# Kernel tuning notes

Measured on AMD Instinct MI355X. Metric: run time of the kernel, lower is better.

The kernel has to match this reference:

```python
import jax, jax.numpy as jnp
import numpy as np

EMB, HID, SEQ, BATCH, VOCAB, LAYERS = 1024, 1024, 128, 64, 10000, 2


def setup_inputs() -> dict:
    key = jax.random.key(0)
    ks = jax.random.split(key, 10)
    k = 1.0 / np.sqrt(HID)
    u = lambda kk, shape, lo, hi: jax.random.uniform(kk, shape, jnp.float32, lo, hi)
    return {
        "inputs": jax.random.randint(ks[0], (SEQ, BATCH), 0, VOCAB, jnp.int32),
        "hidden": jnp.zeros((LAYERS, BATCH, HID), jnp.float32),
        "embedding": u(ks[1], (VOCAB, EMB), -0.1, 0.1),
        "wx0": u(ks[2], (HID, EMB), -k, k),
        "wh0": u(ks[3], (HID, HID), -k, k),
        "bh0": u(ks[4], (HID,), -k, k),
        "wx1": u(ks[5], (HID, HID), -k, k),
        "wh1": u(ks[6], (HID, HID), -k, k),
        "bh1": u(ks[7], (HID,), -k, k),
        "v_w": u(ks[8], (VOCAB, HID), -0.1, 0.1),
        "v_b": jnp.zeros((VOCAB,), jnp.float32),
    }


def reference(inputs, hidden, embedding, wx0, wh0, bh0, wx1, wh1, bh1, v_w, v_b):
    # dropout is identity (dp_keep_prob = 1.0)
    emb = embedding[inputs]  # (S, B, E)

    def step(h, x_t):
        # h: (L, B, H); x_t: (B, E)
        h0 = jnp.tanh(x_t @ wx0.T + h[0] @ wh0.T + bh0)
        h1 = jnp.tanh(h0 @ wx1.T + h[1] @ wh1.T + bh1)
        return jnp.stack([h0, h1]), h1

    hidden_final, top = jax.lax.scan(step, hidden, emb)  # top: (S, B, H)
    logits = jnp.einsum("sbh,vh->sbv", top, v_w) + v_b  # (S, B, V)
    return logits, hidden_final
```

## Files before the change

kernel.cpp:

```cpp
#include <hip/hip_runtime.h>
#include <stdint.h>

typedef __attribute__((ext_vector_type(8))) short short8;
typedef __attribute__((ext_vector_type(4))) float f32x4;
typedef __attribute__((ext_vector_type(4))) unsigned short ushort4v;
typedef __attribute__((ext_vector_type(4))) float float4v;

#define DEVFN static __device__ __forceinline__
#define SPIN_CAP (1u << 20)

DEVFN unsigned short f32_to_bf16_rn(float x) {
  unsigned u = __builtin_bit_cast(unsigned, x);
  unsigned r = u + 0x7FFFu + ((u >> 16) & 1u);
  return (unsigned short)(r >> 16);
}
DEVFN float bf16_to_f32(unsigned short h) {
  unsigned u = ((unsigned)h) << 16;
  return __builtin_bit_cast(float, u);
}

__global__ void k_split(const float* __restrict__ src, unsigned short* __restrict__ hi,
                        unsigned short* __restrict__ lo, int n) {
  int i = (blockIdx.x * 256 + threadIdx.x) * 4;
  if (i >= n) return;
  float4v v = *reinterpret_cast<const float4v*>(src + i);
  ushort4v h, l;
#pragma unroll
  for (int j = 0; j < 4; ++j) {
    unsigned short hb = f32_to_bf16_rn(v[j]);
    float rem = v[j] - bf16_to_f32(hb);
    h[j] = hb;
    l[j] = f32_to_bf16_rn(rem);
  }
  *reinterpret_cast<ushort4v*>(hi + i) = h;
  *reinterpret_cast<ushort4v*>(lo + i) = l;
}

__global__ void k_embed(const int* __restrict__ tok, const float* __restrict__ emb,
                        unsigned short* __restrict__ hi, unsigned short* __restrict__ lo) {
  int m = blockIdx.x;
  int t = tok[m];
  const float* row = emb + (size_t)t * 1024;
  int e = threadIdx.x * 4;
  float4v v = *reinterpret_cast<const float4v*>(row + e);
  ushort4v h, l;
#pragma unroll
  for (int j = 0; j < 4; ++j) {
    unsigned short hb = f32_to_bf16_rn(v[j]);
    float rem = v[j] - bf16_to_f32(hb);
    h[j] = hb;
    l[j] = f32_to_bf16_rn(rem);
  }
  *reinterpret_cast<ushort4v*>(hi + (size_t)m * 1024 + e) = h;
  *reinterpret_cast<ushort4v*>(lo + (size_t)m * 1024 + e) = l;
}

template <bool NGUARD>
__global__ __launch_bounds__(256) void k_gemm_nt(
    const unsigned short* __restrict__ Ahi, const unsigned short* __restrict__ Alo,
    const unsigned short* __restrict__ Bhi, const unsigned short* __restrict__ Blo,
    float* __restrict__ C, const float* __restrict__ bias, int N) {
  const int K = 1024;
  __shared__ unsigned short sA[2][128][40];
  __shared__ unsigned short sB[2][128][40];
  const int m0 = blockIdx.y * 128;
  const int n0 = blockIdx.x * 128;
  const int tid = threadIdx.x;
  const int lane = tid & 63, wave = tid >> 6;
  const int wm = (wave >> 1) * 64, wn = (wave & 1) * 64;
  const int fr = lane & 15, fk = (lane >> 4) * 8, fm = (lane >> 4) * 4;

  f32x4 acc[4][4] = {};

  for (int k0 = 0; k0 < K; k0 += 32) {
    __syncthreads();
#pragma unroll
    for (int a = 0; a < 2; ++a) {
      const unsigned short* As = a ? Alo : Ahi;
      const unsigned short* Bs = a ? Blo : Bhi;
#pragma unroll
      for (int p = 0; p < 2; ++p) {
        int seg = p * 256 + tid;
        int row = seg >> 2, sk = (seg & 3) * 8;
        short8 va = *reinterpret_cast<const short8*>(As + (size_t)(m0 + row) * K + k0 + sk);
        *reinterpret_cast<short8*>(&sA[a][row][sk]) = va;
        short8 vb;
        if (!NGUARD || (n0 + row) < N)
          vb = *reinterpret_cast<const short8*>(Bs + (size_t)(n0 + row) * K + k0 + sk);
        else
          vb = short8{0, 0, 0, 0, 0, 0, 0, 0};
        *reinterpret_cast<short8*>(&sB[a][row][sk]) = vb;
      }
    }
    __syncthreads();

    short8 afh[4], afl[4], bfh[4], bfl[4];
#pragma unroll
    for (int i = 0; i < 4; ++i) {
      afh[i] = *reinterpret_cast<const short8*>(&sA[0][wm + i * 16 + fr][fk]);
      afl[i] = *reinterpret_cast<const short8*>(&sA[1][wm + i * 16 + fr][fk]);
      bfh[i] = *reinterpret_cast<const short8*>(&sB[0][wn + i * 16 + fr][fk]);
      bfl[i] = *reinterpret_cast<const short8*>(&sB[1][wn + i * 16 + fr][fk]);
    }
#pragma unroll
    for (int i = 0; i < 4; ++i)
#pragma unroll
      for (int j = 0; j < 4; ++j) {
        acc[i][j] = __builtin_amdgcn_mfma_f32_16x16x32_bf16(afh[i], bfh[j], acc[i][j], 0, 0, 0);
        acc[i][j] = __builtin_amdgcn_mfma_f32_16x16x32_bf16(afl[i], bfh[j], acc[i][j], 0, 0, 0);
        acc[i][j] = __builtin_amdgcn_mfma_f32_16x16x32_bf16(afh[i], bfl[j], acc[i][j], 0, 0, 0);
      }
  }

#pragma unroll
  for (int i = 0; i < 4; ++i)
#pragma unroll
    for (int j = 0; j < 4; ++j) {
      int n = n0 + wn + j * 16 + fr;
      if (NGUARD && n >= N) continue;
      float bv = bias[n];
#pragma unroll
      for (int r = 0; r < 4; ++r) {
        int m = m0 + wm + i * 16 + fm + r;
        C[(size_t)m * N + n] = acc[i][j][r] + bv;
      }
    }
}

#define NWG_L0 32
#define NWG_CMP 96

DEVFN f32x4 MFMA(short8 a, short8 b, f32x4 c) {
  return __builtin_amdgcn_mfma_f32_16x16x32_bf16(a, b, c, 0, 0, 0);
}

__global__ __launch_bounds__(256, 1) void k_rnn_fused(
    const float* __restrict__ X0,
    unsigned short* __restrict__ H0hi, unsigned short* __restrict__ H0lo,
    unsigned short* __restrict__ H1hi, unsigned short* __restrict__ H1lo,
    const unsigned short* __restrict__ Wh0hi, const unsigned short* __restrict__ Wh0lo,
    const unsigned short* __restrict__ Wx1hi, const unsigned short* __restrict__ Wx1lo,
    const unsigned short* __restrict__ Wh1hi, const unsigned short* __restrict__ Wh1lo,
    const float* __restrict__ bh1,
    unsigned* __restrict__ slots, unsigned* __restrict__ release) {
  const int wg = blockIdx.x;
  const int tid = threadIdx.x;

  if (wg == NWG_CMP) {
    if (tid >= 64) return;
    const int lane = tid;
    for (int i = 0; i < 129; ++i) {
      unsigned want = (unsigned)(i + 1);
      for (unsigned sp = 0; sp < SPIN_CAP; ++sp) {
        unsigned a = __hip_atomic_load(&slots[lane * 32], __ATOMIC_RELAXED,
                                       __HIP_MEMORY_SCOPE_AGENT);
        unsigned b = (lane < 32) ? __hip_atomic_load(&slots[(64 + lane) * 32], __ATOMIC_RELAXED,
                                                     __HIP_MEMORY_SCOPE_AGENT)
                                 : 0xFFFFFFFFu;
        if (__all(a >= want && b >= want)) break;
        __builtin_amdgcn_s_sleep(1);
      }
      if (lane == 0)
        __hip_atomic_store(release, want, __ATOMIC_RELAXED, __HIP_MEMORY_SCOPE_AGENT);
    }
    return;
  }

  const int lane = tid & 63, kw = tid >> 6;
  const int fr = lane & 15, fk = (lane >> 4) * 8;
  const int pr = (lane >> 4) * 4;
  const bool isL0 = wg < NWG_L0;
  __shared__ float red[4][64][36];

  short8 bh_[2][8], bl_[2][8];
  int n0;
  if (isL0) {
    n0 = wg * 32;
#pragma unroll
    for (int cf = 0; cf < 2; ++cf)
#pragma unroll
      for (int ch = 0; ch < 8; ++ch) {
        size_t off = (size_t)(n0 + cf * 16 + fr) * 1024 + kw * 256 + ch * 32 + fk;
        bh_[cf][ch] = *reinterpret_cast<const short8*>(Wh0hi + off);
        bl_[cf][ch] = *reinterpret_cast<const short8*>(Wh0lo + off);
      }
  } else {
    n0 = (wg - NWG_L0) * 16;
#pragma unroll
    for (int ch = 0; ch < 8; ++ch) {
      size_t off = (size_t)(n0 + fr) * 1024 + kw * 256 + ch * 32 + fk;
      bh_[0][ch] = *reinterpret_cast<const short8*>(Wx1hi + off);
      bl_[0][ch] = *reinterpret_cast<const short8*>(Wx1lo + off);
      bh_[1][ch] = *reinterpret_cast<const short8*>(Wh1hi + off);
      bl_[1][ch] = *reinterpret_cast<const short8*>(Wh1lo + off);
    }
  }
  float bias1[4];
  if (!isL0) {
    int cb = (tid & 3) * 4;
#pragma unroll
    for (int c = 0; c < 4; ++c) bias1[c] = bh1[n0 + cb + c];
  }

  for (int i = 0; i <= 128; ++i) {
    const bool active = isL0 ? (i < 128) : (i >= 1);
    if (active) {
      if (isL0) {
        const unsigned short* ah = H0hi + (size_t)i * 65536;
        const unsigned short* al = H0lo + (size_t)i * 65536;
        f32x4 acc[4][2] = {};
#pragma unroll
        for (int ch = 0; ch < 8; ++ch) {
          short8 Ah[4], Al[4];
#pragma unroll
          for (int rf = 0; rf < 4; ++rf) {
            size_t off = (size_t)(rf * 16 + fr) * 1024 + kw * 256 + ch * 32 + fk;
            Ah[rf] = *reinterpret_cast<const short8*>(ah + off);
            Al[rf] = *reinterpret_cast<const short8*>(al + off);
          }
#pragma unroll
          for (int rf = 0; rf < 4; ++rf)
#pragma unroll
            for (int cf = 0; cf < 2; ++cf) {
              acc[rf][cf] = MFMA(Ah[rf], bh_[cf][ch], acc[rf][cf]);
              acc[rf][cf] = MFMA(Al[rf], bh_[cf][ch], acc[rf][cf]);
              acc[rf][cf] = MFMA(Ah[rf], bl_[cf][ch], acc[rf][cf]);
            }
        }
#pragma unroll
        for (int rf = 0; rf < 4; ++rf)
#pragma unroll
          for (int cf = 0; cf < 2; ++cf)
#pragma unroll
            for (int r = 0; r < 4; ++r)
              red[kw][rf * 16 + pr + r][cf * 16 + fr] = acc[rf][cf][r];
      } else {
        const unsigned short* a0h = H0hi + (size_t)i * 65536;
        const unsigned short* a0l = H0lo + (size_t)i * 65536;
        const unsigned short* a1h = H1hi + (size_t)(i - 1) * 65536;
        const unsigned short* a1l = H1lo + (size_t)(i - 1) * 65536;
        f32x4 acc0[4] = {}, acc1[4] = {};
#pragma unroll
        for (int ch = 0; ch < 8; ++ch) {
          short8 A0h[4], A0l[4], A1h[4], A1l[4];
#pragma unroll
          for (int rf = 0; rf < 4; ++rf) {
            size_t off = (size_t)(rf * 16 + fr) * 1024 + kw * 256 + ch * 32 + fk;
            A0h[rf] = *reinterpret_cast<const short8*>(a0h + off);
            A0l[rf] = *reinterpret_cast<const short8*>(a0l + off);
            A1h[rf] = *reinterpret_cast<const short8*>(a1h + off);
            A1l[rf] = *reinterpret_cast<const short8*>(a1l + off);
          }
#pragma unroll
          for (int rf = 0; rf < 4; ++rf) {
            acc0[rf] = MFMA(A0h[rf], bh_[0][ch], acc0[rf]);
            acc0[rf] = MFMA(A0l[rf], bh_[0][ch], acc0[rf]);
            acc0[rf] = MFMA(A0h[rf], bl_[0][ch], acc0[rf]);
            acc1[rf] = MFMA(A1h[rf], bh_[1][ch], acc1[rf]);
            acc1[rf] = MFMA(A1l[rf], bh_[1][ch], acc1[rf]);
            acc1[rf] = MFMA(A1h[rf], bl_[1][ch], acc1[rf]);
          }
        }
#pragma unroll
        for (int rf = 0; rf < 4; ++rf)
#pragma unroll
          for (int r = 0; r < 4; ++r)
            red[kw][rf * 16 + pr + r][fr] = acc0[rf][r] + acc1[rf][r];
      }
      __syncthreads();
      if (isL0) {
        int row = tid >> 2, cb = (tid & 3) * 8;
        const float* Xt = X0 + (size_t)i * 65536 + (size_t)row * 1024 + n0;
        size_t ob = (size_t)(i + 1) * 65536 + (size_t)row * 1024 + n0;
#pragma unroll
        for (int c = 0; c < 8; ++c) {
          int col = cb + c;
          float s = red[0][row][col] + red[1][row][col] + red[2][row][col] + red[3][row][col];
          float val = tanhf(Xt[col] + s);
          unsigned short hb = f32_to_bf16_rn(val);
          float rem = val - bf16_to_f32(hb);
          __hip_atomic_store(H0hi + ob + col, hb, __ATOMIC_RELAXED, __HIP_MEMORY_SCOPE_AGENT);
          __hip_atomic_store(H0lo + ob + col, f32_to_bf16_rn(rem), __ATOMIC_RELAXED,
                             __HIP_MEMORY_SCOPE_AGENT);
        }
      } else {
        int row = tid >> 2, cb = (tid & 3) * 4;
        size_t ob = (size_t)i * 65536 + (size_t)row * 1024 + n0;
#pragma unroll
        for (int c = 0; c < 4; ++c) {
          int col = cb + c;
          float s = red[0][row][col] + red[1][row][col] + red[2][row][col] + red[3][row][col];
          float val = tanhf(bias1[c] + s);
          unsigned short hb = f32_to_bf16_rn(val);
          float rem = val - bf16_to_f32(hb);
          __hip_atomic_store(H1hi + ob + col, hb, __ATOMIC_RELAXED, __HIP_MEMORY_SCOPE_AGENT);
          __hip_atomic_store(H1lo + ob + col, f32_to_bf16_rn(rem), __ATOMIC_RELAXED,
                             __HIP_MEMORY_SCOPE_AGENT);
        }
      }
    }
    __syncthreads();
    if (tid == 0) {
      __hip_atomic_store(&slots[wg * 32], (unsigned)(i + 1), __ATOMIC_RELAXED,
                         __HIP_MEMORY_SCOPE_AGENT);
      for (unsigned sp = 0; sp < SPIN_CAP; ++sp) {
        if (__hip_atomic_load(release, __ATOMIC_RELAXED, __HIP_MEMORY_SCOPE_AGENT) >=
            (unsigned)(i + 1))
          break;
        __builtin_amdgcn_s_sleep(1);
      }
    }
    __syncthreads();
  }
}

__global__ void k_hidfinal(const unsigned short* __restrict__ H0hi,
                           const unsigned short* __restrict__ H0lo,
                           const unsigned short* __restrict__ H1hi,
                           const unsigned short* __restrict__ H1lo,
                           float* __restrict__ out) {
  size_t i = (size_t)blockIdx.x * 256 + threadIdx.x;
  const size_t off = (size_t)128 * 65536;
  out[i] = bf16_to_f32(H0hi[off + i]) + bf16_to_f32(H0lo[off + i]);
  out[65536 + i] = bf16_to_f32(H1hi[off + i]) + bf16_to_f32(H1lo[off + i]);
}

extern "C" void kernel_launch(void* const* d_in, const int* in_sizes, int n_in,
                              void* d_out, int out_size, void* d_ws, size_t ws_size,
                              hipStream_t stream) {
  const int* inputs = (const int*)d_in[0];
  const float* hidden = (const float*)d_in[1];
  const float* emb = (const float*)d_in[2];
  const float* wx0 = (const float*)d_in[3];
  const float* wh0 = (const float*)d_in[4];
  const float* bh0 = (const float*)d_in[5];
  const float* wx1 = (const float*)d_in[6];
  const float* wh1 = (const float*)d_in[7];
  const float* bh1 = (const float*)d_in[8];
  const float* v_w = (const float*)d_in[9];
  const float* v_b = (const float*)d_in[10];
  float* out = (float*)d_out;

  char* ws = (char*)d_ws;
  size_t off = 0;
  auto alloc = [&](size_t bytes) -> char* {
    char* p = ws + off;
    off += (bytes + 255) & ~(size_t)255;
    return p;
  };
  const size_t WB = (size_t)1024 * 1024 * 2;
  unsigned short* wx0hi = (unsigned short*)alloc(WB);
  unsigned short* wx0lo = (unsigned short*)alloc(WB);
  unsigned short* wh0hi = (unsigned short*)alloc(WB);
  unsigned short* wh0lo = (unsigned short*)alloc(WB);
  unsigned short* wx1hi = (unsigned short*)alloc(WB);
  unsigned short* wx1lo = (unsigned short*)alloc(WB);
  unsigned short* wh1hi = (unsigned short*)alloc(WB);
  unsigned short* wh1lo = (unsigned short*)alloc(WB);
  unsigned short* vwhi = (unsigned short*)alloc((size_t)10000 * 1024 * 2);
  unsigned short* vwlo = (unsigned short*)alloc((size_t)10000 * 1024 * 2);
  unsigned short* aehi = (unsigned short*)alloc((size_t)8192 * 1024 * 2);
  unsigned short* aelo = (unsigned short*)alloc((size_t)8192 * 1024 * 2);
  float* X0 = (float*)alloc((size_t)8192 * 1024 * 4);
  const size_t HS = (size_t)129 * 65536 * 2;
  unsigned short* H0hi = (unsigned short*)alloc(HS);
  unsigned short* H0lo = (unsigned short*)alloc(HS);
  unsigned short* H1hi = (unsigned short*)alloc(HS);
  unsigned short* H1lo = (unsigned short*)alloc(HS);
  unsigned* barbuf = (unsigned*)alloc(16384);
  unsigned* slots = barbuf;
  unsigned* release = barbuf + 100 * 32;

  k_split<<<1024, 256, 0, stream>>>(wx0, wx0hi, wx0lo, 1024 * 1024);
  k_split<<<1024, 256, 0, stream>>>(wh0, wh0hi, wh0lo, 1024 * 1024);
  k_split<<<1024, 256, 0, stream>>>(wx1, wx1hi, wx1lo, 1024 * 1024);
  k_split<<<1024, 256, 0, stream>>>(wh1, wh1hi, wh1lo, 1024 * 1024);
  k_split<<<10000, 256, 0, stream>>>(v_w, vwhi, vwlo, 10000 * 1024);
  k_split<<<64, 256, 0, stream>>>(hidden, H0hi, H0lo, 65536);
  k_split<<<64, 256, 0, stream>>>(hidden + 65536, H1hi, H1lo, 65536);
  k_embed<<<8192, 256, 0, stream>>>(inputs, emb, aehi, aelo);
  hipMemsetAsync(barbuf, 0, 16384, stream);

  dim3 g1(8, 64);
  k_gemm_nt<false><<<g1, 256, 0, stream>>>(aehi, aelo, wx0hi, wx0lo, X0, bh0, 1024);

  k_rnn_fused<<<97, 256, 0, stream>>>(X0, H0hi, H0lo, H1hi, H1lo, wh0hi, wh0lo, wx1hi, wx1lo,
                                      wh1hi, wh1lo, bh1, slots, release);

  dim3 g3(79, 64);
  k_gemm_nt<true><<<g3, 256, 0, stream>>>(H1hi + 65536, H1lo + 65536, vwhi, vwlo, out, v_b, 10000);
  k_hidfinal<<<256, 256, 0, stream>>>(H0hi, H0lo, H1hi, H1lo, out + (size_t)81920000);
}
```

Before: 3.704 ms.

## Spread persistent RNN across more workgroups with 8-way K split and sharded release flags

The persistent recurrent kernel grows from 97 to 129 workgroups of 512 threads. Each layer-0 workgroup now owns 16 output columns instead of 32, and K is split across 8 waves instead of 4, so each wave keeps less weight data in registers and does less serial work per step. The single release flag becomes 8 padded copies so pollers are spread across cache lines, and sleep intervals change. The epilogue now packs two bf16 values per 32-bit atomic store. The cost is a larger 8-way LDS reduction and a barrier that has to collect more workgroups each step.

```diff
diff --git a/kernel.cpp b/kernel.cpp
--- a/kernel.cpp
+++ b/kernel.cpp
@@ -5,6 +5,7 @@
 typedef __attribute__((ext_vector_type(4))) float f32x4;
 typedef __attribute__((ext_vector_type(4))) unsigned short ushort4v;
 typedef __attribute__((ext_vector_type(4))) float float4v;
+typedef __attribute__((ext_vector_type(2))) float float2v;
 
 #define DEVFN static __device__ __forceinline__
 #define SPIN_CAP (1u << 20)
@@ -18,6 +19,7 @@
   unsigned u = ((unsigned)h) << 16;
   return __builtin_bit_cast(float, u);
 }
+DEVFN void pin(short8& x) { asm volatile("" : "+v"(*reinterpret_cast<f32x4*>(&x))); }
 
 __global__ void k_split(const float* __restrict__ src, unsigned short* __restrict__ hi,
                         unsigned short* __restrict__ lo, int n) {
@@ -127,14 +129,14 @@
     }
 }
 
-#define NWG_L0 32
-#define NWG_CMP 96
+#define NWG_L0 64
+#define WG_CHK 128
 
 DEVFN f32x4 MFMA(short8 a, short8 b, f32x4 c) {
   return __builtin_amdgcn_mfma_f32_16x16x32_bf16(a, b, c, 0, 0, 0);
 }
 
-__global__ __launch_bounds__(256, 1) void k_rnn_fused(
+__global__ __launch_bounds__(512, 2) void k_rnn_fused(
     const float* __restrict__ X0,
     unsigned short* __restrict__ H0hi, unsigned short* __restrict__ H0lo,
     unsigned short* __restrict__ H1hi, unsigned short* __restrict__ H1lo,
@@ -142,11 +144,11 @@
     const unsigned short* __restrict__ Wx1hi, const unsigned short* __restrict__ Wx1lo,
     const unsigned short* __restrict__ Wh1hi, const unsigned short* __restrict__ Wh1lo,
     const float* __restrict__ bh1,
-    unsigned* __restrict__ slots, unsigned* __restrict__ release) {
+    unsigned* __restrict__ slots, unsigned* __restrict__ releases) {
   const int wg = blockIdx.x;
   const int tid = threadIdx.x;
 
-  if (wg == NWG_CMP) {
+  if (wg == WG_CHK) {
     if (tid >= 64) return;
     const int lane = tid;
     for (int i = 0; i < 129; ++i) {
@@ -154,14 +156,14 @@
       for (unsigned sp = 0; sp < SPIN_CAP; ++sp) {
         unsigned a = __hip_atomic_load(&slots[lane * 32], __ATOMIC_RELAXED,
                                        __HIP_MEMORY_SCOPE_AGENT);
-        unsigned b = (lane < 32) ? __hip_atomic_load(&slots[(64 + lane) * 32], __ATOMIC_RELAXED,
-                                                     __HIP_MEMORY_SCOPE_AGENT)
-                                 : 0xFFFFFFFFu;
+        unsigned b = __hip_atomic_load(&slots[(64 + lane) * 32], __ATOMIC_RELAXED,
+                                       __HIP_MEMORY_SCOPE_AGENT);
         if (__all(a >= want && b >= want)) break;
-        __builtin_amdgcn_s_sleep(1);
-      }
-      if (lane == 0)
-        __hip_atomic_store(release, want, __ATOMIC_RELAXED, __HIP_MEMORY_SCOPE_AGENT);
+        __builtin_amdgcn_s_sleep(2);
+      }
+      if (lane < 8)
+        __hip_atomic_store(&releases[lane * 32], want, __ATOMIC_RELAXED,
+                           __HIP_MEMORY_SCOPE_AGENT);
     }
     return;
   }
@@ -170,82 +172,76 @@
   const int fr = lane & 15, fk = (lane >> 4) * 8;
   const int pr = (lane >> 4) * 4;
   const bool isL0 = wg < NWG_L0;
-  __shared__ float red[4][64][36];
-
-  short8 bh_[2][8], bl_[2][8];
-  int n0;
+  const int n0 = (isL0 ? wg : (wg - NWG_L0)) * 16;
+  __shared__ float red[8][64][20];
+
+  short8 w0h[4], w0l[4], w1h[4], w1l[4];
   if (isL0) {
-    n0 = wg * 32;
-#pragma unroll
-    for (int cf = 0; cf < 2; ++cf)
-#pragma unroll
-      for (int ch = 0; ch < 8; ++ch) {
-        size_t off = (size_t)(n0 + cf * 16 + fr) * 1024 + kw * 256 + ch * 32 + fk;
-        bh_[cf][ch] = *reinterpret_cast<const short8*>(Wh0hi + off);
-        bl_[cf][ch] = *reinterpret_cast<const short8*>(Wh0lo + off);
-      }
+#pragma unroll
+    for (int ch = 0; ch < 4; ++ch) {
+      size_t off = (size_t)(n0 + fr) * 1024 + kw * 128 + ch * 32 + fk;
+      w0h[ch] = *reinterpret_cast<const short8*>(Wh0hi + off);
+      w0l[ch] = *reinterpret_cast<const short8*>(Wh0lo + off);
+      pin(w0h[ch]); pin(w0l[ch]);
+    }
   } else {
-    n0 = (wg - NWG_L0) * 16;
-#pragma unroll
-    for (int ch = 0; ch < 8; ++ch) {
-      size_t off = (size_t)(n0 + fr) * 1024 + kw * 256 + ch * 32 + fk;
-      bh_[0][ch] = *reinterpret_cast<const short8*>(Wx1hi + off);
-      bl_[0][ch] = *reinterpret_cast<const short8*>(Wx1lo + off);
-      bh_[1][ch] = *reinterpret_cast<const short8*>(Wh1hi + off);
-      bl_[1][ch] = *reinterpret_cast<const short8*>(Wh1lo + off);
-    }
-  }
-  float bias1[4];
+#pragma unroll
+    for (int ch = 0; ch < 4; ++ch) {
+      size_t off = (size_t)(n0 + fr) * 1024 + kw * 128 + ch * 32 + fk;
+      w0h[ch] = *reinterpret_cast<const short8*>(Wx1hi + off);
+      w0l[ch] = *reinterpret_cast<const short8*>(Wx1lo + off);
+      w1h[ch] = *reinterpret_cast<const short8*>(Wh1hi + off);
+      w1l[ch] = *reinterpret_cast<const short8*>(Wh1lo + off);
+      pin(w0h[ch]); pin(w0l[ch]); pin(w1h[ch]); pin(w1l[ch]);
+    }
+  }
+  const int row = tid >> 3;
+  const int c0 = (tid & 7) * 2;
+  float bias0 = 0.f, bias1v = 0.f;
   if (!isL0) {
-    int cb = (tid & 3) * 4;
-#pragma unroll
-    for (int c = 0; c < 4; ++c) bias1[c] = bh1[n0 + cb + c];
+    bias0 = bh1[n0 + c0];
+    bias1v = bh1[n0 + c0 + 1];
   }
 
   for (int i = 0; i <= 128; ++i) {
     const bool active = isL0 ? (i < 128) : (i >= 1);
     if (active) {
       if (isL0) {
-        const unsigned short* ah = H0hi + (size_t)i * 65536;
-        const unsigned short* al = H0lo + (size_t)i * 65536;
-        f32x4 acc[4][2] = {};
-#pragma unroll
-        for (int ch = 0; ch < 8; ++ch) {
+        const unsigned short* ah = H0hi + (size_t)i * 65536 + kw * 128 + fk;
+        const unsigned short* al = H0lo + (size_t)i * 65536 + kw * 128 + fk;
+        f32x4 acc[4] = {};
+#pragma unroll
+        for (int ch = 0; ch < 4; ++ch) {
           short8 Ah[4], Al[4];
 #pragma unroll
           for (int rf = 0; rf < 4; ++rf) {
-            size_t off = (size_t)(rf * 16 + fr) * 1024 + kw * 256 + ch * 32 + fk;
+            size_t off = (size_t)(rf * 16 + fr) * 1024 + ch * 32;
             Ah[rf] = *reinterpret_cast<const short8*>(ah + off);
             Al[rf] = *reinterpret_cast<const short8*>(al + off);
           }
 #pragma unroll
-          for (int rf = 0; rf < 4; ++rf)
-#pragma unroll
-            for (int cf = 0; cf < 2; ++cf) {
-              acc[rf][cf] = MFMA(Ah[rf], bh_[cf][ch], acc[rf][cf]);
-              acc[rf][cf] = MFMA(Al[rf], bh_[cf][ch], acc[rf][cf]);
-              acc[rf][cf] = MFMA(Ah[rf], bl_[cf][ch], acc[rf][cf]);
-            }
+          for (int rf = 0; rf < 4; ++rf) {
+            acc[rf] = MFMA(Ah[rf], w0h[ch], acc[rf]);
+            acc[rf] = MFMA(Al[rf], w0h[ch], acc[rf]);
+            acc[rf] = MFMA(Ah[rf], w0l[ch], acc[rf]);
+          }
         }
 #pragma unroll
         for (int rf = 0; rf < 4; ++rf)
 #pragma unroll
-          for (int cf = 0; cf < 2; ++cf)
-#pragma unroll
-            for (int r = 0; r < 4; ++r)
-              red[kw][rf * 16 + pr + r][cf * 16 + fr] = acc[rf][cf][r];
+          for (int r = 0; r < 4; ++r) red[kw][rf * 16 + pr + r][fr] = acc[rf][r];
       } else {
-        const unsigned short* a0h = H0hi + (size_t)i * 65536;
-        const unsigned short* a0l = H0lo + (size_t)i * 65536;
-        const unsigned short* a1h = H1hi + (size_t)(i - 1) * 65536;
-        const unsigned short* a1l = H1lo + (size_t)(i - 1) * 65536;
+        const unsigned short* a0h = H0hi + (size_t)i * 65536 + kw * 128 + fk;
+        const unsigned short* a0l = H0lo + (size_t)i * 65536 + kw * 128 + fk;
+        const unsigned short* a1h = H1hi + (size_t)(i - 1) * 65536 + kw * 128 + fk;
+        const unsigned short* a1l = H1lo + (size_t)(i - 1) * 65536 + kw * 128 + fk;
         f32x4 acc0[4] = {}, acc1[4] = {};
 #pragma unroll
-        for (int ch = 0; ch < 8; ++ch) {
+        for (int ch = 0; ch < 4; ++ch) {
           short8 A0h[4], A0l[4], A1h[4], A1l[4];
 #pragma unroll
           for (int rf = 0; rf < 4; ++rf) {
-            size_t off = (size_t)(rf * 16 + fr) * 1024 + kw * 256 + ch * 32 + fk;
+            size_t off = (size_t)(rf * 16 + fr) * 1024 + ch * 32;
             A0h[rf] = *reinterpret_cast<const short8*>(a0h + off);
             A0l[rf] = *reinterpret_cast<const short8*>(a0l + off);
             A1h[rf] = *reinterpret_cast<const short8*>(a1h + off);
@@ -253,12 +249,12 @@
           }
 #pragma unroll
           for (int rf = 0; rf < 4; ++rf) {
-            acc0[rf] = MFMA(A0h[rf], bh_[0][ch], acc0[rf]);
-            acc0[rf] = MFMA(A0l[rf], bh_[0][ch], acc0[rf]);
-            acc0[rf] = MFMA(A0h[rf], bl_[0][ch], acc0[rf]);
-            acc1[rf] = MFMA(A1h[rf], bh_[1][ch], acc1[rf]);
-            acc1[rf] = MFMA(A1l[rf], bh_[1][ch], acc1[rf]);
-            acc1[rf] = MFMA(A1h[rf], bl_[1][ch], acc1[rf]);
+            acc0[rf] = MFMA(A0h[rf], w0h[ch], acc0[rf]);
+            acc0[rf] = MFMA(A0l[rf], w0h[ch], acc0[rf]);
+            acc0[rf] = MFMA(A0h[rf], w0l[ch], acc0[rf]);
+            acc1[rf] = MFMA(A1h[rf], w1h[ch], acc1[rf]);
+            acc1[rf] = MFMA(A1l[rf], w1h[ch], acc1[rf]);
+            acc1[rf] = MFMA(A1h[rf], w1l[ch], acc1[rf]);
           }
         }
 #pragma unroll
@@ -268,46 +264,46 @@
             red[kw][rf * 16 + pr + r][fr] = acc0[rf][r] + acc1[rf][r];
       }
       __syncthreads();
+      float s0 = 0.f, s1 = 0.f;
+#pragma unroll
+      for (int k8 = 0; k8 < 8; ++k8) {
+        s0 += red[k8][row][c0];
+        s1 += red[k8][row][c0 + 1];
+      }
+      float v0, v1;
+      size_t ob;
       if (isL0) {
-        int row = tid >> 2, cb = (tid & 3) * 8;
-        const float* Xt = X0 + (size_t)i * 65536 + (size_t)row * 1024 + n0;
-        size_t ob = (size_t)(i + 1) * 65536 + (size_t)row * 1024 + n0;
-#pragma unroll
-        for (int c = 0; c < 8; ++c) {
-          int col = cb + c;
-          float s = red[0][row][col] + red[1][row][col] + red[2][row][col] + red[3][row][col];
-          float val = tanhf(Xt[col] + s);
-          unsigned short hb = f32_to_bf16_rn(val);
-          float rem = val - bf16_to_f32(hb);
-          __hip_atomic_store(H0hi + ob + col, hb, __ATOMIC_RELAXED, __HIP_MEMORY_SCOPE_AGENT);
-          __hip_atomic_store(H0lo + ob + col, f32_to_bf16_rn(rem), __ATOMIC_RELAXED,
-                             __HIP_MEMORY_SCOPE_AGENT);
-        }
+        const float* Xt = X0 + (size_t)i * 65536 + (size_t)row * 1024 + n0 + c0;
+        v0 = tanhf(Xt[0] + s0);
+        v1 = tanhf(Xt[1] + s1);
+        ob = (size_t)(i + 1) * 65536 + (size_t)row * 1024 + n0 + c0;
       } else {
-        int row = tid >> 2, cb = (tid & 3) * 4;
-        size_t ob = (size_t)i * 65536 + (size_t)row * 1024 + n0;
-#pragma unroll
-        for (int c = 0; c < 4; ++c) {
-          int col = cb + c;
-          float s = red[0][row][col] + red[1][row][col] + red[2][row][col] + red[3][row][col];
-          float val = tanhf(bias1[c] + s);
-          unsigned short hb = f32_to_bf16_rn(val);
-          float rem = val - bf16_to_f32(hb);
-          __hip_atomic_store(H1hi + ob + col, hb, __ATOMIC_RELAXED, __HIP_MEMORY_SCOPE_AGENT);
-          __hip_atomic_store(H1lo + ob + col, f32_to_bf16_rn(rem), __ATOMIC_RELAXED,
-                             __HIP_MEMORY_SCOPE_AGENT);
-        }
-      }
+        v0 = tanhf(bias0 + s0);
+        v1 = tanhf(bias1v + s1);
+        ob = (size_t)i * 65536 + (size_t)row * 1024 + n0 + c0;
+      }
+      unsigned short hb0 = f32_to_bf16_rn(v0), hb1 = f32_to_bf16_rn(v1);
+      unsigned short lb0 = f32_to_bf16_rn(v0 - bf16_to_f32(hb0));
+      unsigned short lb1 = f32_to_bf16_rn(v1 - bf16_to_f32(hb1));
+      unsigned uhi = (unsigned)hb0 | ((unsigned)hb1 << 16);
+      unsigned ulo = (unsigned)lb0 | ((unsigned)lb1 << 16);
+      unsigned short* dh = isL0 ? H0hi : H1hi;
+      unsigned short* dl = isL0 ? H0lo : H1lo;
+      __hip_atomic_store(reinterpret_cast<unsigned*>(dh + ob), uhi, __ATOMIC_RELAXED,
+                         __HIP_MEMORY_SCOPE_AGENT);
+      __hip_atomic_store(reinterpret_cast<unsigned*>(dl + ob), ulo, __ATOMIC_RELAXED,
+                         __HIP_MEMORY_SCOPE_AGENT);
     }
     __syncthreads();
     if (tid == 0) {
       __hip_atomic_store(&slots[wg * 32], (unsigned)(i + 1), __ATOMIC_RELAXED,
                          __HIP_MEMORY_SCOPE_AGENT);
+      unsigned* myrel = &releases[(wg & 7) * 32];
       for (unsigned sp = 0; sp < SPIN_CAP; ++sp) {
-        if (__hip_atomic_load(release, __ATOMIC_RELAXED, __HIP_MEMORY_SCOPE_AGENT) >=
+        if (__hip_atomic_load(myrel, __ATOMIC_RELAXED, __HIP_MEMORY_SCOPE_AGENT) >=
             (unsigned)(i + 1))
           break;
-        __builtin_amdgcn_s_sleep(1);
+        __builtin_amdgcn_s_sleep(4);
       }
     }
     __syncthreads();
@@ -367,9 +363,9 @@
   unsigned short* H0lo = (unsigned short*)alloc(HS);
   unsigned short* H1hi = (unsigned short*)alloc(HS);
   unsigned short* H1lo = (unsigned short*)alloc(HS);
-  unsigned* barbuf = (unsigned*)alloc(16384);
+  unsigned* barbuf = (unsigned*)alloc(32768);
   unsigned* slots = barbuf;
-  unsigned* release = barbuf + 100 * 32;
+  unsigned* releases = barbuf + 4096;
 
   k_split<<<1024, 256, 0, stream>>>(wx0, wx0hi, wx0lo, 1024 * 1024);
   k_split<<<1024, 256, 0, stream>>>(wh0, wh0hi, wh0lo, 1024 * 1024);
@@ -379,13 +375,13 @@
   k_split<<<64, 256, 0, stream>>>(hidden, H0hi, H0lo, 65536);
   k_split<<<64, 256, 0, stream>>>(hidden + 65536, H1hi, H1lo, 65536);
   k_embed<<<8192, 256, 0, stream>>>(inputs, emb, aehi, aelo);
-  hipMemsetAsync(barbuf, 0, 16384, stream);
+  hipMemsetAsync(barbuf, 0, 32768, stream);
 
   dim3 g1(8, 64);
   k_gemm_nt<false><<<g1, 256, 0, stream>>>(aehi, aelo, wx0hi, wx0lo, X0, bh0, 1024);
 
-  k_rnn_fused<<<97, 256, 0, stream>>>(X0, H0hi, H0lo, H1hi, H1lo, wh0hi, wh0lo, wx1hi, wx1lo,
-                                      wh1hi, wh1lo, bh1, slots, release);
+  k_rnn_fused<<<129, 512, 0, stream>>>(X0, H0hi, H0lo, H1hi, H1lo, wh0hi, wh0lo, wx1hi, wx1lo,
+                                       wh1hi, wh1lo, bh1, slots, releases);
 
   dim3 g3(79, 64);
   k_gemm_nt<true><<<g3, 256, 0, stream>>>(H1hi + 65536, H1lo + 65536, vwhi, vwlo, out, v_b, 10000);
```

After: 3.273 ms. 1.13x faster.
